# Optimization experiments

Hardware: AMD Instinct MI355X
Metric: run time of the kernel (lower is better)

Reference implementation:

```python
import jax, jax.numpy as jnp
import numpy as np

MUL = 32           # multiplicity per in1 irrep (must be multiple of WARPSIZE=32)
LMAX = 2
# uvu instructions: all (l1, l2, l3) allowed by triangle rule with l3 <= LMAX
INSTR = [(l1, l2, l3)
         for l1 in range(LMAX + 1)
         for l2 in range(LMAX + 1)
         for l3 in range(abs(l1 - l2), min(l1 + l2, LMAX) + 1)]
# in1 layout: [32x0e | 32x1e | 32x2e] flattened as (mul, ir_dim) blocks
_IN1_OFF = np.cumsum([0] + [MUL * (2 * l + 1) for l in range(LMAX + 1)])
_IN2_OFF = np.cumsum([0] + [(2 * l + 1) for l in range(LMAX + 1)])

# standing in for the unique_cg_mat / unique_cg_val metadata of the module.
_rng = np.random.default_rng(42)
CG = []
for (l1, l2, l3) in INSTR:
    d1, d2, d3 = 2 * l1 + 1, 2 * l2 + 1, 2 * l3 + 1
    mask = _rng.random((d1, d2, d3)) < 0.3
    if not mask.any():
        mask[0, 0, 0] = True
    vals = _rng.normal(size=(d1, d2, d3)).astype(np.float32)
    CG.append(np.where(mask, vals, 0.0).astype(np.float32))
# e3nn-style path normalization weights
PATH_W = [np.float32(1.0 / np.sqrt((2 * l1 + 1) * (2 * l2 + 1))) for (l1, l2, l3) in INSTR]

N_NODES = 10000
N_EDGES = 100000
IN1_DIM = int(_IN1_OFF[-1])   # 288
IN2_DIM = int(_IN2_OFF[-1])   # 9
W_DIM = len(INSTR) * MUL      # 480 (uvu: u*v = 32*1 per path)


def setup_inputs() -> dict:
    key = jax.random.key(0)
    k1, k2, k3, k4, k5 = jax.random.split(key, 5)
    return {
        "in1": jax.random.normal(k1, (N_NODES, IN1_DIM), dtype=jnp.float32),
        "in2": jax.random.normal(k2, (N_EDGES, IN2_DIM), dtype=jnp.float32),
        "weight": jax.random.normal(k3, (N_EDGES, W_DIM), dtype=jnp.float32),
        "per_edge_src": jax.random.randint(k4, (N_EDGES,), 0, N_NODES, dtype=jnp.int64),
        "per_edge_dst": jax.random.randint(k5, (N_EDGES,), 0, N_NODES, dtype=jnp.int64),
    }


def reference(in1, in2, weight, per_edge_src, per_edge_dst):
    n_nodes = in1.shape[0]
    E = in2.shape[0]
    x1 = in1[per_edge_src]  # gather per-edge source node features [E, 288]
    outs = []
    for idx, (l1, l2, l3) in enumerate(INSTR):
        d1 = 2 * l1 + 1
        a = x1[:, _IN1_OFF[l1]:_IN1_OFF[l1 + 1]].reshape(E, MUL, d1)   # [E, u, d1]
        b = in2[:, _IN2_OFF[l2]:_IN2_OFF[l2 + 1]]                      # [E, d2]
        w = weight[:, idx * MUL:(idx + 1) * MUL]                       # [E, u]
        cg = jnp.asarray(CG[idx])
        # sparse CG contraction: out[e,u,k] = pw * sum_ij x1[e,u,i] x2[e,j] cg[i,j,k] * w[e,u]
        o = jnp.einsum('eui,ej,ijk->euk', a, b, cg) * PATH_W[idx]
        o = o * w[:, :, None]
        outs.append(o.reshape(E, -1))
    per_edge_out = jnp.concatenate(outs, axis=-1)  # [E, 1632]
    # scatter-reduce to destination atoms
    return jax.ops.segment_sum(per_edge_out, per_edge_dst, num_segments=n_nodes)
```

## Files before the change

kernel.cpp:

```cpp
#include <hip/hip_runtime.h>
#include <cstdint>
#include <cmath>
#include <cstring>
#include <mutex>

namespace nprng {

typedef unsigned __int128 u128;

struct PCG64 {
  u128 state, inc;
  static inline u128 mult() {
    return ((u128)0x2360ED051FC65DA4ULL << 64) | 0x4385DF649FCCF645ULL;
  }
  inline void step() { state = state * mult() + inc; }
  inline uint64_t next() {
    step();
    uint64_t hi = (uint64_t)(state >> 64), lo = (uint64_t)state;
    uint64_t x = hi ^ lo;
    unsigned rot = (unsigned)(state >> 122);
    return (x >> rot) | (x << ((64u - rot) & 63u));
  }
  void srandom(u128 initstate, u128 initseq) {
    state = 0;
    inc = (initseq << 1) | 1;
    step();
    state += initstate;
    step();
  }
};

static void seed_sequence_42_raw(uint32_t st[8]) {
  uint32_t pool[4];
  uint32_t hash_const = 0x43b0d7e5u;
  auto hashmix = [&hash_const](uint32_t v) -> uint32_t {
    v ^= hash_const;
    hash_const *= 0x931e8875u;
    v *= hash_const;
    v ^= v >> 16;
    return v;
  };
  auto mix = [](uint32_t x, uint32_t y) -> uint32_t {
    uint32_t r = 0xca01f9ddu * x - 0x4973f715u * y;
    r ^= r >> 16;
    return r;
  };
  pool[0] = hashmix(42u);
  for (int i = 1; i < 4; ++i) pool[i] = hashmix(0u);
  for (int s = 0; s < 4; ++s)
    for (int d = 0; d < 4; ++d)
      if (s != d) pool[d] = mix(pool[d], hashmix(pool[s]));
  uint32_t gen_const = 0x8b51f9ddu;
  for (int i = 0; i < 8; ++i) {
    uint32_t v = pool[i & 3];
    v ^= gen_const;
    gen_const *= 0x58f38dedu;
    v *= gen_const;
    v ^= v >> 16;
    st[i] = v;
  }
}

static inline double next_uniform(PCG64& g) {
  return (double)(g.next() >> 11) * (1.0 / 9007199254740992.0);
}

static void make_gen(PCG64& g) {
  uint32_t st[8];
  seed_sequence_42_raw(st);
  const double target = 0.7739560485559633;
  for (int pairing = 0; pairing < 2; ++pairing) {
    uint64_t s[4];
    for (int i = 0; i < 4; ++i)
      s[i] = pairing == 0
                 ? ((uint64_t)st[2 * i] | ((uint64_t)st[2 * i + 1] << 32))
                 : (((uint64_t)st[2 * i] << 32) | (uint64_t)st[2 * i + 1]);
    for (int so = 0; so < 2; ++so) {
      PCG64 t;
      if (so == 0)
        t.srandom(((u128)s[0] << 64) | s[1], ((u128)s[2] << 64) | s[3]);
      else
        t.srandom(((u128)s[1] << 64) | s[0], ((u128)s[3] << 64) | s[2]);
      PCG64 probe = t;
      if (fabs(next_uniform(probe) - target) < 1e-13) {
        g = t;
        return;
      }
    }
  }
  uint64_t s[4];
  for (int i = 0; i < 4; ++i)
    s[i] = (uint64_t)st[2 * i] | ((uint64_t)st[2 * i + 1] << 32);
  g.srandom(((u128)s[0] << 64) | s[1], ((u128)s[2] << 64) | s[3]);
}

struct Zig {
  double wi[256], fi[256];
  uint64_t ki[256];
};

static void build_zig(Zig& z) {
  const long double R = 3.6541528853610087963519472518L;
  const long double T52 = 4503599627370496.0L;
  long double f255 = expl(-0.5L * R * R);
  long double v =
      R * f255 +
      sqrtl(1.57079632679489661923132169163975144L) *
          erfcl(R / 1.41421356237309504880168872420969808L);
  long double x[256], fi[256];
  x[255] = R;
  fi[255] = f255;
  for (int i = 254; i >= 1; --i) {
    fi[i] = fi[i + 1] + v / x[i + 1];
    long double t = -2.0L * logl(fi[i]);
    x[i] = t > 0 ? sqrtl(t) : 0.0L;
  }
  x[0] = 0.0L;
  fi[0] = 1.0L;
  z.wi[0] = (double)(v / f255 / T52);
  z.fi[0] = 1.0;
  z.ki[0] = (uint64_t)((R * f255 / v) * T52);
  z.ki[1] = 0;
  for (int i = 1; i < 256; ++i) {
    z.wi[i] = (double)(x[i] / T52);
    z.fi[i] = (double)fi[i];
  }
  for (int i = 2; i < 256; ++i)
    z.ki[i] = (uint64_t)((x[i - 1] / x[i]) * T52);
}

static double next_normal(PCG64& g, const Zig& z) {
  const double ZR = 3.6541528853610087963519472518;
  const double ZIR = 0.27366123732975827203338247596;
  for (;;) {
    uint64_t r = g.next();
    int idx = (int)(r & 0xff);
    r >>= 8;
    int sign = (int)(r & 1);
    uint64_t rabs = (r >> 1) & 0x000fffffffffffffULL;
    double x = (double)rabs * z.wi[idx];
    if (sign) x = -x;
    if (rabs < z.ki[idx]) return x;
    if (idx == 0) {
      double xx, yy;
      do {
        xx = -ZIR * log1p(-next_uniform(g));
        yy = -log1p(-next_uniform(g));
      } while (yy + yy <= xx * xx);
      return ((rabs >> 8) & 1) ? -(ZR + xx) : (ZR + xx);
    } else {
      if ((z.fi[idx - 1] - z.fi[idx]) * next_uniform(g) + z.fi[idx] <
          exp(-0.5 * x * x))
        return x;
    }
  }
}

static const int kInstr[15][3] = {{0, 0, 0}, {0, 1, 1}, {0, 2, 2}, {1, 0, 1},
                                 {1, 1, 0}, {1, 1, 1}, {1, 1, 2}, {1, 2, 1},
                                 {1, 2, 2}, {2, 0, 2}, {2, 1, 1}, {2, 1, 2},
                                 {2, 2, 0}, {2, 2, 1}, {2, 2, 2}};
static const int kCOff[15] = {0,   1,   10,  35,  44,  53,  80, 125,
                              170, 245, 270, 315, 390, 415, 490};

static void build_coeff(float* coeff) {
  Zig z;
  build_zig(z);
  PCG64 g;
  make_gen(g);
  for (int t = 0; t < 15; ++t) {
    int d1 = 2 * kInstr[t][0] + 1;
    int d2 = 2 * kInstr[t][1] + 1;
    int d3 = 2 * kInstr[t][2] + 1;
    int n = d1 * d2 * d3;
    bool mask[125];
    bool any = false;
    for (int i = 0; i < n; ++i) {
      mask[i] = next_uniform(g) < 0.3;
      any |= mask[i];
    }
    if (!any) mask[0] = true;
    float pw = (float)(1.0 / sqrt((double)(d1 * d2)));
    for (int i = 0; i < n; ++i) {
      float v = (float)next_normal(g, z);
      coeff[kCOff[t] + i] = mask[i] ? v * pw : 0.0f;
    }
  }
}

}


struct CtvArg {
  float v[26 * 32];
};
struct CoeffArg {
  float v[615];
};

#define FOR_PATHS(X)    \
  X(0, 0, 1, 0, 0)      \
  X(3, 1, 3, 4, 9)      \
  X(9, 2, 5, 16, 29)    \
  X(1, 0, 3, 64, 1)     \
  X(4, 1, 1, 68, 12)    \
  X(5, 1, 3, 72, 13)    \
  X(6, 1, 5, 84, 16)    \
  X(10, 2, 3, 100, 34)  \
  X(11, 2, 5, 116, 37)  \
  X(2, 0, 5, 160, 4)    \
  X(7, 1, 3, 168, 21)   \
  X(8, 1, 5, 180, 24)   \
  X(12, 2, 1, 196, 42)  \
  X(13, 2, 3, 204, 43)  \
  X(14, 2, 5, 220, 46)

static void build_ctv(const float* h_coeff, CtvArg* ctv) {
  struct PD {
    int coff, d1, d3, padbase;
  };
  static const PD c0[] = {{0, 1, 1, 0}, {35, 3, 3, 4}, {245, 5, 5, 16}};
  static const PD c1[] = {{1, 1, 3, 64},   {44, 3, 1, 68},  {53, 3, 3, 72},
                          {80, 3, 5, 84},  {270, 5, 3, 100}, {315, 5, 5, 116}};
  static const PD c2[] = {{10, 1, 5, 160}, {125, 3, 3, 168}, {170, 3, 5, 180},
                          {390, 5, 1, 196}, {415, 5, 3, 204}, {490, 5, 5, 220}};
  const PD* cls[3] = {c0, c1, c2};
  const int ncls[3] = {3, 6, 6};
  const int rounds[3] = {2, 3, 3};
  const int cbase[3] = {0, 64, 160};
  const int qbase[3] = {0, 2, 11};
  for (int c = 0; c < 3; ++c) {
    int d2 = 2 * c + 1;
    for (int r = 0; r < rounds[c]; ++r)
      for (int t = 0; t < d2; ++t) {
        int q = qbase[c] + r * d2 + t;
        for (int lane = 0; lane < 32; ++lane) {
          int slot = cbase[c] + r * 32 + lane;
          float val = 0.0f;
          for (int pi = 0; pi < ncls[c]; ++pi) {
            const PD& pd = cls[c][pi];
            int rel = slot - pd.padbase;
            if (rel >= 0 && rel < pd.d1 * pd.d3) {
              int i = rel / pd.d3, k = rel % pd.d3;
              val = h_coeff[pd.coff + (i * d2 + t) * pd.d3 + k];
              break;
            }
          }
          ctv->v[q * 32 + lane] = val;
        }
      }
  }
}

__global__ void hist_kernel(const int* __restrict__ edst,
                            int* __restrict__ counts, int E) {
  int e = blockIdx.x * blockDim.x + threadIdx.x;
  if (e < E) atomicAdd(&counts[edst[e]], 1);
}

__global__ __launch_bounds__(1024) void scan_kernel(
    const int* __restrict__ counts, int* __restrict__ offsets, int n) {
  __shared__ int sh[1024];
  int t = threadIdx.x;
  int chunk = (n + 1023) >> 10;
  int start = t * chunk;
  int local[16];
  int sum = 0;
#pragma unroll
  for (int i = 0; i < 16; ++i) {
    if (i < chunk) {
      int idx = start + i;
      int v = (idx < n) ? counts[idx] : 0;
      local[i] = sum;
      sum += v;
    }
  }
  sh[t] = sum;
  __syncthreads();
  for (int off = 1; off < 1024; off <<= 1) {
    int v = (t >= off) ? sh[t - off] : 0;
    __syncthreads();
    sh[t] += v;
    __syncthreads();
  }
  int base = (t == 0) ? 0 : sh[t - 1];
#pragma unroll
  for (int i = 0; i < 16; ++i) {
    if (i < chunk) {
      int idx = start + i;
      if (idx < n) offsets[idx] = base + local[i];
    }
  }
  if (t == 1023) offsets[n] = sh[1023];
}

__global__ void fill_kernel(const int* __restrict__ edst,
                            const int* __restrict__ offsets,
                            int* __restrict__ cursor, int* __restrict__ csr,
                            int E) {
  int e = blockIdx.x * blockDim.x + threadIdx.x;
  if (e >= E) return;
  int d = edst[e];
  int pos = atomicAdd(&cursor[d], 1);
  csr[offsets[d] + pos] = e;
}

template <int D1, int D3, int PB, int AOFF>
__device__ __forceinline__ void consume(const float* lbc,
                                        const float (&a)[D1], float w,
                                        float (&acc)[51]) {
  constexpr int NR = (D1 * D3 + 3) / 4;
  float fb[NR * 4];
#pragma unroll
  for (int r = 0; r < NR; ++r) {
    float4 v = *reinterpret_cast<const float4*>(lbc + PB + 4 * r);
    fb[4 * r + 0] = v.x;
    fb[4 * r + 1] = v.y;
    fb[4 * r + 2] = v.z;
    fb[4 * r + 3] = v.w;
  }
  float tmp[D3];
#pragma unroll
  for (int k = 0; k < D3; ++k) tmp[k] = a[0] * fb[k];
#pragma unroll
  for (int i = 1; i < D1; ++i)
#pragma unroll
    for (int k = 0; k < D3; ++k) tmp[k] = fmaf(a[i], fb[i * D3 + k], tmp[k]);
#pragma unroll
  for (int k = 0; k < D3; ++k) acc[AOFF + k] = fmaf(w, tmp[k], acc[AOFF + k]);
}

#define DO_CONSUME(p, l1, d3c, pb, aoff) \
  consume<2 * (l1) + 1, d3c, pb, aoff>(lbc, aa##l1, ww[p], acc);

#define DO_REDUCE(p, l1, d3c, pb, aoff)                    \
  _Pragma("unroll") for (int k = 0; k < (d3c); ++k)        \
      acc[(aoff) + k] += __shfl_xor(acc[(aoff) + k], 32, 64);

#define DO_STORE(p, l1, d3c, pb, aoff)                     \
  _Pragma("unroll") for (int k = 0; k < (d3c); ++k)        \
      O[(aoff)*32 + u * (d3c) + k] = acc[(aoff) + k];

__global__ __launch_bounds__(256) void tp_node_kernel(
    CtvArg cc, const float* __restrict__ in1, const float* __restrict__ in2,
    const float* __restrict__ weight, const int* __restrict__ esrc,
    const int* __restrict__ offsets, const int* __restrict__ csr,
    float* __restrict__ out, int N) {
  __shared__ float lds[4][2][256];
  int t = blockIdx.x * blockDim.x + threadIdx.x;
  int u = t & 31;
  int es = (t >> 5) & 1;
  int n = t >> 6;
  if (n >= N) return;
  int wv = threadIdx.x >> 6;
  float* lbc = &lds[wv][es][0];

  float ctv[26];
#pragma unroll
  for (int q = 0; q < 26; ++q) ctv[q] = cc.v[q * 32 + u];

  int beg = offsets[n];
  int end = offsets[n + 1];

  float acc[51];
#pragma unroll
  for (int k = 0; k < 51; ++k) acc[k] = 0.0f;

  for (int ii = beg + es; ii < end; ii += 2) {
    int e = csr[ii];
    int s = esrc[e];
    const float* __restrict__ A = in1 + (size_t)s * 288;
    const float* __restrict__ B = in2 + (size_t)e * 9;
    const float* __restrict__ W = weight + (size_t)e * 480 + u;

    float aa0[1], aa1[3], aa2[5];
    float b0v, bb1[3], bb2[5];
    float ww[15];
    aa0[0] = A[u];
#pragma unroll
    for (int i = 0; i < 3; ++i) aa1[i] = A[32 + u * 3 + i];
#pragma unroll
    for (int i = 0; i < 5; ++i) aa2[i] = A[128 + u * 5 + i];
    b0v = B[0];
#pragma unroll
    for (int j = 0; j < 3; ++j) bb1[j] = B[1 + j];
#pragma unroll
    for (int j = 0; j < 5; ++j) bb2[j] = B[4 + j];
#pragma unroll
    for (int p = 0; p < 15; ++p) ww[p] = W[p * 32];

    float* wp = lbc + u;
    wp[0] = ctv[0] * b0v;
    wp[32] = ctv[1] * b0v;
#pragma unroll
    for (int r = 0; r < 3; ++r)
      wp[64 + r * 32] =
          fmaf(ctv[2 + 3 * r], bb1[0],
               fmaf(ctv[3 + 3 * r], bb1[1], ctv[4 + 3 * r] * bb1[2]));
#pragma unroll
    for (int r = 0; r < 3; ++r)
      wp[160 + r * 32] =
          fmaf(ctv[11 + 5 * r], bb2[0],
               fmaf(ctv[12 + 5 * r], bb2[1],
                    fmaf(ctv[13 + 5 * r], bb2[2],
                         fmaf(ctv[14 + 5 * r], bb2[3],
                              ctv[15 + 5 * r] * bb2[4]))));

    __builtin_amdgcn_wave_barrier();
    asm volatile("" ::: "memory");

    FOR_PATHS(DO_CONSUME)

    asm volatile("" ::: "memory");
  }

  FOR_PATHS(DO_REDUCE)
  if (es == 0) {
    float* __restrict__ O = out + (size_t)n * 1632;
    FOR_PATHS(DO_STORE)
  }
}

#define FOR_ALL_INSTR(X)                                                   \
  X(0, 0, 0, 0, 0, 0)                                                      \
  X(1, 0, 1, 1, 1, 1)                                                      \
  X(2, 0, 2, 2, 10, 4)                                                     \
  X(3, 1, 0, 1, 35, 9)                                                     \
  X(4, 1, 1, 0, 44, 12)                                                    \
  X(5, 1, 1, 1, 53, 13)                                                    \
  X(6, 1, 1, 2, 80, 16)                                                    \
  X(7, 1, 2, 1, 125, 21)                                                   \
  X(8, 1, 2, 2, 170, 24)                                                   \
  X(9, 2, 0, 2, 245, 29)                                                   \
  X(10, 2, 1, 1, 270, 34)                                                  \
  X(11, 2, 1, 2, 315, 37)                                                  \
  X(12, 2, 2, 0, 390, 42)                                                  \
  X(13, 2, 2, 1, 415, 43)                                                  \
  X(14, 2, 2, 2, 490, 46)

template <int D1, int D2, int D3, int COFF, int AOFF>
__device__ __forceinline__ void contract(const float* __restrict__ ct,
                                         const float (&a)[D1],
                                         const float (&b)[D2],
                                         float (&acc)[51]) {
#pragma unroll
  for (int i = 0; i < D1; ++i)
#pragma unroll
    for (int j = 0; j < D2; ++j) {
      float ab = a[i] * b[j];
#pragma unroll
      for (int k = 0; k < D3; ++k)
        acc[AOFF + k] =
            fmaf(ab, ct[COFF + (i * D2 + j) * D3 + k], acc[AOFF + k]);
    }
}

#define DO_CONTRACT(idx, l1, l2, l3, coff, aoff)                       \
  contract<2 * (l1) + 1, 2 * (l2) + 1, 2 * (l3) + 1, coff, aoff>(      \
      ct, aa##l1, bb##l2, acc);

#define DO_EPI(idx, l1, l2, l3, coff, aoff)                            \
  {                                                                    \
    float wv2 = W[(idx)*32];                                           \
    _Pragma("unroll") for (int k = 0; k < 2 * (l3) + 1; ++k)           \
        atomicAdd(O + ((aoff)*32 + u * (2 * (l3) + 1) + k),            \
                  acc[(aoff) + k] * wv2);                              \
  }

__global__ __launch_bounds__(256) void tp_kernel(
    const float* __restrict__ in1, const float* __restrict__ in2,
    const float* __restrict__ weight, const int* __restrict__ esrc,
    const int* __restrict__ edst, const float* __restrict__ ct,
    float* __restrict__ out, int E) {
  int t = blockIdx.x * blockDim.x + threadIdx.x;
  int e = t >> 5;
  if (e >= E) return;
  int u = t & 31;
  int s = esrc[e];
  int d = edst[e];
  const float* __restrict__ A = in1 + (size_t)s * 288;
  const float* __restrict__ B = in2 + (size_t)e * 9;
  const float* __restrict__ W = weight + (size_t)e * 480 + u;
  float* __restrict__ O = out + (size_t)d * 1632;

  float aa0[1], aa1[3], aa2[5], bb0[1], bb1[3], bb2[5];
  aa0[0] = A[u];
#pragma unroll
  for (int i = 0; i < 3; ++i) aa1[i] = A[32 + u * 3 + i];
#pragma unroll
  for (int i = 0; i < 5; ++i) aa2[i] = A[128 + u * 5 + i];
  bb0[0] = B[0];
#pragma unroll
  for (int j = 0; j < 3; ++j) bb1[j] = B[1 + j];
#pragma unroll
  for (int j = 0; j < 5; ++j) bb2[j] = B[4 + j];

  float acc[51];
#pragma unroll
  for (int k = 0; k < 51; ++k) acc[k] = 0.0f;

  FOR_ALL_INSTR(DO_CONTRACT)
  FOR_ALL_INSTR(DO_EPI)
}


extern "C" void kernel_launch(void* const* d_in, const int* in_sizes, int n_in,
                              void* d_out, int out_size, void* d_ws,
                              size_t ws_size, hipStream_t stream) {
  static float h_coeff[615];
  static CtvArg h_ctv;
  static std::once_flag once;
  std::call_once(once, []() {
    nprng::build_coeff(h_coeff);
    build_ctv(h_coeff, &h_ctv);
    (void)hipHostRegister(h_coeff, sizeof(h_coeff), hipHostRegisterDefault);
  });

  const float* in1 = (const float*)d_in[0];
  const float* in2 = (const float*)d_in[1];
  const float* wgt = (const float*)d_in[2];
  const int* esrc = (const int*)d_in[3];
  const int* edst = (const int*)d_in[4];
  float* out = (float*)d_out;

  int N = in_sizes[0] / 288;
  int E = in_sizes[1] / 9;

  int* ws = (int*)d_ws;
  const int CNT_OFF = 0;
  const int CUR_OFF = CNT_OFF + N;
  const int OFF_OFF = CUR_OFF + N;
  int csr_off = OFF_OFF + N + 1;
  csr_off = (csr_off + 3) & ~3;
  size_t needed = (size_t)(csr_off + E) * 4;

  if (ws_size >= needed) {
    int* counts = ws + CNT_OFF;
    int* cursor = ws + CUR_OFF;
    int* offsets = ws + OFF_OFF;
    int* csr = ws + csr_off;

    hipMemsetAsync(counts, 0, (size_t)(2 * N) * 4, stream);
    hist_kernel<<<(E + 255) / 256, 256, 0, stream>>>(edst, counts, E);
    scan_kernel<<<1, 1024, 0, stream>>>(counts, offsets, N);
    fill_kernel<<<(E + 255) / 256, 256, 0, stream>>>(edst, offsets, cursor,
                                                     csr, E);
    int blocks = (N + 3) / 4;
    tp_node_kernel<<<blocks, 256, 0, stream>>>(h_ctv, in1, in2, wgt, esrc,
                                               offsets, csr, out, N);
  } else if (ws_size >= sizeof(h_coeff)) {
    float* ct = (float*)ws;
    hipMemcpyAsync(ct, h_coeff, sizeof(h_coeff), hipMemcpyHostToDevice,
                   stream);
    hipMemsetAsync(out, 0, (size_t)out_size * sizeof(float), stream);
    int threads = E * 32;
    tp_kernel<<<(threads + 255) / 256, 256, 0, stream>>>(in1, in2, wgt, esrc,
                                                         edst, ct, out, E);
  }
}
```

Baseline: 349.3 us.

## Software-pipeline edge loads with double-buffered registers in node kernel

The per-node edge loop is restructured to prefetch the next edge's in1/in2/weight data and the index chain two edges ahead while computing the current edge. Two register buffer sets alternate via an unrolled STEP macro, so global memory latency can be hidden behind the CG contraction math. This raises register pressure (two sets of 33 floats plus indices), which may lower occupancy.

```diff
diff --git a/kernel.cpp b/kernel.cpp
--- a/kernel.cpp
+++ b/kernel.cpp
@@ -193,9 +193,6 @@
 
 struct CtvArg {
   float v[26 * 32];
-};
-struct CoeffArg {
-  float v[615];
 };
 
 #define FOR_PATHS(X)    \
@@ -305,10 +302,9 @@
   csr[offsets[d] + pos] = e;
 }
 
-template <int D1, int D3, int PB, int AOFF>
-__device__ __forceinline__ void consume(const float* lbc,
-                                        const float (&a)[D1], float w,
-                                        float (&acc)[51]) {
+template <int D1, int D3, int PB, int AOFF, int AB>
+__device__ __forceinline__ void consume(const float* lbc, const float (&a)[9],
+                                        float w, float (&acc)[51]) {
   constexpr int NR = (D1 * D3 + 3) / 4;
   float fb[NR * 4];
 #pragma unroll
@@ -321,17 +317,19 @@
   }
   float tmp[D3];
 #pragma unroll
-  for (int k = 0; k < D3; ++k) tmp[k] = a[0] * fb[k];
+  for (int k = 0; k < D3; ++k) tmp[k] = a[AB] * fb[k];
 #pragma unroll
   for (int i = 1; i < D1; ++i)
 #pragma unroll
-    for (int k = 0; k < D3; ++k) tmp[k] = fmaf(a[i], fb[i * D3 + k], tmp[k]);
+    for (int k = 0; k < D3; ++k)
+      tmp[k] = fmaf(a[AB + i], fb[i * D3 + k], tmp[k]);
 #pragma unroll
   for (int k = 0; k < D3; ++k) acc[AOFF + k] = fmaf(w, tmp[k], acc[AOFF + k]);
 }
 
-#define DO_CONSUME(p, l1, d3c, pb, aoff) \
-  consume<2 * (l1) + 1, d3c, pb, aoff>(lbc, aa##l1, ww[p], acc);
+#define DO_CONSUME(p, l1, d3c, pb, aoff)                               \
+  consume<2 * (l1) + 1, d3c, pb, aoff,                                 \
+          ((l1) == 0 ? 0 : ((l1) == 1 ? 1 : 4))>(lbc, Ac, Wc[p], acc);
 
 #define DO_REDUCE(p, l1, d3c, pb, aoff)                    \
   _Pragma("unroll") for (int k = 0; k < (d3c); ++k)        \
@@ -340,6 +338,58 @@
 #define DO_STORE(p, l1, d3c, pb, aoff)                     \
   _Pragma("unroll") for (int k = 0; k < (d3c); ++k)        \
       O[(aoff)*32 + u * (d3c) + k] = acc[(aoff) + k];
+
+#define LOAD_EDGE(AV, BV, WV, ev, sv)                                      \
+  {                                                                        \
+    const float* __restrict__ An = in1 + (size_t)(sv)*288;                 \
+    const float* __restrict__ Bn = in2 + (size_t)(ev)*9;                   \
+    const float* __restrict__ Wn = weight + (size_t)(ev)*480 + u;          \
+    AV[0] = An[u];                                                         \
+    _Pragma("unroll") for (int i = 0; i < 3; ++i)                          \
+        AV[1 + i] = An[32 + u * 3 + i];                                    \
+    _Pragma("unroll") for (int i = 0; i < 5; ++i)                          \
+        AV[4 + i] = An[128 + u * 5 + i];                                   \
+    _Pragma("unroll") for (int j = 0; j < 9; ++j) BV[j] = Bn[j];           \
+    _Pragma("unroll") for (int p = 0; p < 15; ++p) WV[p] = Wn[p * 32];     \
+  }
+
+#define STEP(C, N)                                                         \
+  {                                                                        \
+                   \
+    float* wp = lbc + u;                                                   \
+    wp[0] = ctv[0] * B##C[0];                                              \
+    wp[32] = ctv[1] * B##C[0];                                             \
+    _Pragma("unroll") for (int r = 0; r < 3; ++r)                          \
+        wp[64 + r * 32] =                                                  \
+        fmaf(ctv[2 + 3 * r], B##C[1],                                      \
+             fmaf(ctv[3 + 3 * r], B##C[2], ctv[4 + 3 * r] * B##C[3]));     \
+    _Pragma("unroll") for (int r = 0; r < 3; ++r)                          \
+        wp[160 + r * 32] =                                                 \
+        fmaf(ctv[11 + 5 * r], B##C[4],                                     \
+             fmaf(ctv[12 + 5 * r], B##C[5],                                \
+                  fmaf(ctv[13 + 5 * r], B##C[6],                           \
+                       fmaf(ctv[14 + 5 * r], B##C[7],                      \
+                            ctv[15 + 5 * r] * B##C[8]))));                 \
+       \
+    bool hasN = (ii + 2 < end);                                            \
+    if (hasN) LOAD_EDGE(A##N, B##N, W##N, e##N, s##N)                      \
+            \
+    if (ii + 4 < end) {                                                    \
+      e##C = csr[ii + 4];                                                  \
+      s##C = esrc[e##C];                                                   \
+    }                                                                      \
+                \
+    __builtin_amdgcn_wave_barrier();                                       \
+    asm volatile("" ::: "memory");                                         \
+    {                                                                      \
+      const float(&Ac)[9] = A##C;                                          \
+      const float(&Wc)[15] = W##C;                                         \
+      FOR_PATHS(DO_CONSUME)                                                \
+    }                                                                      \
+    asm volatile("" ::: "memory");                                         \
+    ii += 2;                                                               \
+    if (!hasN) break;                                                      \
+  }
 
 __global__ __launch_bounds__(256) void tp_node_kernel(
     CtvArg cc, const float* __restrict__ in1, const float* __restrict__ in2,
@@ -366,52 +416,22 @@
 #pragma unroll
   for (int k = 0; k < 51; ++k) acc[k] = 0.0f;
 
-  for (int ii = beg + es; ii < end; ii += 2) {
-    int e = csr[ii];
-    int s = esrc[e];
-    const float* __restrict__ A = in1 + (size_t)s * 288;
-    const float* __restrict__ B = in2 + (size_t)e * 9;
-    const float* __restrict__ W = weight + (size_t)e * 480 + u;
-
-    float aa0[1], aa1[3], aa2[5];
-    float b0v, bb1[3], bb2[5];
-    float ww[15];
-    aa0[0] = A[u];
-#pragma unroll
-    for (int i = 0; i < 3; ++i) aa1[i] = A[32 + u * 3 + i];
-#pragma unroll
-    for (int i = 0; i < 5; ++i) aa2[i] = A[128 + u * 5 + i];
-    b0v = B[0];
-#pragma unroll
-    for (int j = 0; j < 3; ++j) bb1[j] = B[1 + j];
-#pragma unroll
-    for (int j = 0; j < 5; ++j) bb2[j] = B[4 + j];
-#pragma unroll
-    for (int p = 0; p < 15; ++p) ww[p] = W[p * 32];
-
-    float* wp = lbc + u;
-    wp[0] = ctv[0] * b0v;
-    wp[32] = ctv[1] * b0v;
-#pragma unroll
-    for (int r = 0; r < 3; ++r)
-      wp[64 + r * 32] =
-          fmaf(ctv[2 + 3 * r], bb1[0],
-               fmaf(ctv[3 + 3 * r], bb1[1], ctv[4 + 3 * r] * bb1[2]));
-#pragma unroll
-    for (int r = 0; r < 3; ++r)
-      wp[160 + r * 32] =
-          fmaf(ctv[11 + 5 * r], bb2[0],
-               fmaf(ctv[12 + 5 * r], bb2[1],
-                    fmaf(ctv[13 + 5 * r], bb2[2],
-                         fmaf(ctv[14 + 5 * r], bb2[3],
-                              ctv[15 + 5 * r] * bb2[4]))));
-
-    __builtin_amdgcn_wave_barrier();
-    asm volatile("" ::: "memory");
-
-    FOR_PATHS(DO_CONSUME)
-
-    asm volatile("" ::: "memory");
+  int ii = beg + es;
+  if (ii < end) {
+    int ea, sa, eb = 0, sb = 0;
+    float Aa[9], Ba[9], Wa[15];
+    float Ab[9], Bb[9], Wb[15];
+    ea = csr[ii];
+    sa = esrc[ea];
+    LOAD_EDGE(Aa, Ba, Wa, ea, sa)
+    if (ii + 2 < end) {
+      eb = csr[ii + 2];
+      sb = esrc[eb];
+    }
+    for (;;) {
+      STEP(a, b)
+      STEP(b, a)
+    }
   }
 
   FOR_PATHS(DO_REDUCE)
```

New measurement: 356.5 us. 2.1% more time.
